# Kernel tuning notes

Hardware: AMD Instinct MI355X
Metric: run time of the kernel (lower is better)

The kernel has to match this reference:

```python
import jax, jax.numpy as jnp
import numpy as np

B, S, D, H = 4, 2048, 1024, 16
DK = D // H

def setup_inputs() -> dict:
    key = jax.random.key(0)
    ks = jax.random.split(key, 5)
    x = jax.random.normal(ks[0], (B, S, D), dtype=jnp.float32)
    scale = 1.0 / np.sqrt(D)
    Wq = jax.random.normal(ks[1], (D, D), dtype=jnp.float32) * scale
    Wk = jax.random.normal(ks[2], (D, D), dtype=jnp.float32) * scale
    Wv = jax.random.normal(ks[3], (D, D), dtype=jnp.float32) * scale
    Wo = jax.random.normal(ks[4], (D, D), dtype=jnp.float32) * scale
    return {"x": x, "Wq": Wq, "Wk": Wk, "Wv": Wv, "Wo": Wo}

def reference(x, Wq, Wk, Wv, Wo):
    # F.linear: y = x @ W.T  (weights stored torch-style [out, in])
    q = jnp.einsum('bsd,ed->bse', x, Wq).reshape(B, S, H, DK).transpose(0, 2, 1, 3)
    k = jnp.einsum('bsd,ed->bse', x, Wk).reshape(B, S, H, DK).transpose(0, 2, 1, 3)
    v = jnp.einsum('bsd,ed->bse', x, Wv).reshape(B, S, H, DK).transpose(0, 2, 1, 3)
    scores = jnp.einsum('bhqd,bhkd->bhqk', q, k) / jnp.sqrt(jnp.float32(DK))
    attn = jax.nn.softmax(scores, axis=-1)  # dropout p=0.0 -> identity
    out = jnp.einsum('bhqk,bhkd->bhqd', attn, v)
    out = out.transpose(0, 2, 1, 3).reshape(B, S, D)
    return jnp.einsum('bsd,ed->bse', out, Wo)
```

## Files before the change

kernel.cpp:

```cpp
#include <hip/hip_runtime.h>
#include <hip/hip_bf16.h>

#define B_ 4
#define S_ 2048
#define D_ 1024
#define H_ 16
#define DK_ 64

typedef __attribute__((ext_vector_type(8))) short short8;
typedef __attribute__((ext_vector_type(4))) float floatx4;
typedef __attribute__((ext_vector_type(16))) float floatx16;

static __device__ __forceinline__ unsigned short f2bf(float f) {
    unsigned int u = __float_as_uint(f);
    u += 0x7fffu + ((u >> 16) & 1u);
    return (unsigned short)(u >> 16);
}

static __device__ __forceinline__ unsigned int pack2bf_fast(float a, float b) {
    unsigned int ua = (__float_as_uint(a) + 0x8000u) >> 16;
    unsigned int ub = (__float_as_uint(b) + 0x8000u) & 0xffff0000u;
    return ua | ub;
}

static __device__ __forceinline__ unsigned int pack2bf(float a, float b) {
    return (unsigned int)f2bf(a) | ((unsigned int)f2bf(b) << 16);
}

__global__ void cast_x_kernel(const float* __restrict__ src,
                              unsigned short* __restrict__ dst, int n4) {
    int i = blockIdx.x * blockDim.x + threadIdx.x;
    if (i < n4) {
        float4 v = ((const float4*)src)[i];
        ushort4 o;
        o.x = f2bf(v.x); o.y = f2bf(v.y); o.z = f2bf(v.z); o.w = f2bf(v.w);
        ((ushort4*)dst)[i] = o;
    }
}

struct Ptr4 {
    const float* s[4];
    unsigned short* d[4];
};

__global__ void cast_w_kernel(Ptr4 p, int n4) {
    int m = blockIdx.y;
    int i = blockIdx.x * blockDim.x + threadIdx.x;
    if (i < n4) {
        float4 v = ((const float4*)p.s[m])[i];
        ushort4 o;
        o.x = f2bf(v.x); o.y = f2bf(v.y); o.z = f2bf(v.z); o.w = f2bf(v.w);
        ((ushort4*)p.d[m])[i] = o;
    }
}

template <typename OutT, bool VT2>
__global__ __launch_bounds__(256) void gemm_bt(
    const unsigned short* __restrict__ A,
    const unsigned short* __restrict__ W0,
    const unsigned short* __restrict__ W1,
    const unsigned short* __restrict__ W2,
    OutT* __restrict__ C0, OutT* __restrict__ C1, OutT* __restrict__ C2,
    int M, int N, int K)
{
    __shared__ __align__(16) unsigned short At[128 * 64];
    __shared__ __align__(16) unsigned short Bt[128 * 64];

    const unsigned short* W = (blockIdx.z == 0) ? W0 : ((blockIdx.z == 1) ? W1 : W2);
    OutT* C = (blockIdx.z == 0) ? C0 : ((blockIdx.z == 1) ? C1 : C2);

    const int n0 = blockIdx.x * 128;
    const int m0 = blockIdx.y * 128;
    const int wv = threadIdx.x >> 6;
    const int ln = threadIdx.x & 63;
    const int quad = ln >> 4;
    const int l15 = ln & 15;
    const int wm = (wv >> 1) * 64;
    const int wn = (wv & 1) * 64;

    floatx4 acc[4][4];
#pragma unroll
    for (int i = 0; i < 4; i++)
#pragma unroll
        for (int j = 0; j < 4; j++) acc[i][j] = floatx4{0.f, 0.f, 0.f, 0.f};

    const int lr = ln >> 3;
    const int lc = (ln & 7) * 8;

    for (int k0 = 0; k0 < K; k0 += 64) {
        __syncthreads();
#pragma unroll
        for (int c = 0; c < 4; c++) {
            int rowA = wv * 32 + c * 8;
            const unsigned short* gA = A + (size_t)(m0 + rowA + lr) * K + k0 + lc;
            __builtin_amdgcn_global_load_lds(
                (const __attribute__((address_space(1))) void*)gA,
                (__attribute__((address_space(3))) void*)&At[rowA * 64], 16, 0, 0);
            const unsigned short* gB = W + (size_t)(n0 + rowA + lr) * K + k0 + lc;
            __builtin_amdgcn_global_load_lds(
                (const __attribute__((address_space(1))) void*)gB,
                (__attribute__((address_space(3))) void*)&Bt[rowA * 64], 16, 0, 0);
        }
        __syncthreads();

#pragma unroll
        for (int kk = 0; kk < 2; kk++) {
            short8 af[4], bf[4];
#pragma unroll
            for (int i = 0; i < 4; i++)
                af[i] = *(const short8*)&At[(wm + i * 16 + l15) * 64 + kk * 32 + quad * 8];
#pragma unroll
            for (int j = 0; j < 4; j++)
                bf[j] = *(const short8*)&Bt[(wn + j * 16 + l15) * 64 + kk * 32 + quad * 8];
#pragma unroll
            for (int i = 0; i < 4; i++)
#pragma unroll
                for (int j = 0; j < 4; j++)
                    acc[i][j] = __builtin_amdgcn_mfma_f32_16x16x32_bf16(af[i], bf[j], acc[i][j], 0, 0, 0);
        }
    }

    if constexpr (VT2) {
        if (blockIdx.z == 2) {
            unsigned short* Vt = (unsigned short*)C;
#pragma unroll
            for (int i = 0; i < 4; i++)
#pragma unroll
                for (int j = 0; j < 4; j++) {
                    int col = n0 + wn + j * 16 + l15;
                    int row0 = m0 + wm + i * 16 + quad * 4;
                    int bb = row0 >> 11, ss = row0 & 2047;
                    size_t addr = ((size_t)(bb * 1024 + col)) * 2048 + ss;
                    uint2 pk;
                    pk.x = pack2bf(acc[i][j][0], acc[i][j][1]);
                    pk.y = pack2bf(acc[i][j][2], acc[i][j][3]);
                    *(uint2*)((unsigned short*)Vt + addr) = pk;
                }
            return;
        }
    }

#pragma unroll
    for (int i = 0; i < 4; i++)
#pragma unroll
        for (int j = 0; j < 4; j++)
#pragma unroll
            for (int r = 0; r < 4; r++) {
                int row = m0 + wm + i * 16 + quad * 4 + r;
                int col = n0 + wn + j * 16 + l15;
                float v = acc[i][j][r];
                if constexpr (sizeof(OutT) == 2)
                    C[(size_t)row * N + col] = (OutT)f2bf(v);
                else
                    C[(size_t)row * N + col] = v;
            }
}

__global__ __launch_bounds__(256, 4) void flash_attn(
    const unsigned short* __restrict__ Q,
    const unsigned short* __restrict__ K,
    const unsigned short* __restrict__ Vt,
    unsigned short* __restrict__ O)
{
    __shared__ __align__(16) unsigned short Kt[64 * 72];
    __shared__ __align__(16) unsigned short VT[64 * 72];
    __shared__ __align__(16) unsigned short Pl[4][32 * 72];

    const int qt = blockIdx.x;
    const int h = blockIdx.y;
    const int b = blockIdx.z;
    const int tid = threadIdx.x;
    const int wv = tid >> 6;
    const int ln = tid & 63;
    const int l31 = ln & 31;
    const int half = ln >> 5;

    const size_t base = ((size_t)b * S_) * D_ + (size_t)h * DK_;
    const size_t vtbase = ((size_t)(b * 1024 + h * 64)) * (size_t)S_;

    const int qrow = qt * 128 + wv * 32 + l31;
    short8 qf[4];
    {
        const unsigned short* qp = Q + base + (size_t)qrow * D_ + half * 8;
#pragma unroll
        for (int ks = 0; ks < 4; ks++) qf[ks] = *(const short8*)(qp + ks * 16);
    }

    floatx16 Oacc[2];
#pragma unroll
    for (int mt = 0; mt < 2; mt++)
#pragma unroll
        for (int e = 0; e < 16; e++) Oacc[mt][e] = 0.f;
    float l_i = 0.f;

    const int srow = tid >> 3;
    const int scol = (tid & 7) * 8;

    const float scl = 1.4426950408889634f / 8.0f;
    const float CL = 12.0f;

    for (int kt = 0; kt < S_ / 64; kt++) {
        __syncthreads();
#pragma unroll
        for (int c = 0; c < 2; c++) {
            int row = srow + c * 32;
            *(short8*)&Kt[row * 72 + scol] =
                *(const short8*)(K + base + (size_t)(kt * 64 + row) * D_ + scol);
            *(short8*)&VT[row * 72 + scol] =
                *(const short8*)(Vt + vtbase + (size_t)row * S_ + kt * 64 + scol);
        }
        __syncthreads();

        floatx16 sac[2];
#pragma unroll
        for (int mt = 0; mt < 2; mt++) {
#pragma unroll
            for (int e = 0; e < 16; e++) sac[mt][e] = 0.f;
#pragma unroll
            for (int ks = 0; ks < 4; ks++) {
                short8 kf = *(const short8*)&Kt[(mt * 32 + l31) * 72 + ks * 16 + half * 8];
                sac[mt] = __builtin_amdgcn_mfma_f32_32x32x16_bf16(kf, qf[ks], sac[mt], 0, 0, 0);
            }
        }

#pragma unroll
        for (int mt = 0; mt < 2; mt++)
#pragma unroll
            for (int g = 0; g < 4; g++) {
                float p0 = __builtin_amdgcn_exp2f(fmaf(sac[mt][4 * g + 0], scl, -CL));
                float p1 = __builtin_amdgcn_exp2f(fmaf(sac[mt][4 * g + 1], scl, -CL));
                float p2 = __builtin_amdgcn_exp2f(fmaf(sac[mt][4 * g + 2], scl, -CL));
                float p3 = __builtin_amdgcn_exp2f(fmaf(sac[mt][4 * g + 3], scl, -CL));
                l_i += (p0 + p1) + (p2 + p3);
                uint2 pk;
                pk.x = pack2bf_fast(p0, p1);
                pk.y = pack2bf_fast(p2, p3);
                *(uint2*)&Pl[wv][l31 * 72 + mt * 32 + 8 * g + 4 * half] = pk;
            }
        asm volatile("s_waitcnt lgkmcnt(0)" ::: "memory");

#pragma unroll
        for (int ks = 0; ks < 4; ks++) {
            short8 pf = *(const short8*)&Pl[wv][l31 * 72 + ks * 16 + half * 8];
#pragma unroll
            for (int mt = 0; mt < 2; mt++) {
                short8 vf = *(const short8*)&VT[(mt * 32 + l31) * 72 + ks * 16 + half * 8];
                Oacc[mt] = __builtin_amdgcn_mfma_f32_32x32x16_bf16(vf, pf, Oacc[mt], 0, 0, 0);
            }
        }
    }

    l_i += __shfl_xor(l_i, 32);
    float inv = 1.0f / l_i;

#pragma unroll
    for (int mt = 0; mt < 2; mt++)
#pragma unroll
        for (int g = 0; g < 4; g++) {
            uint2 pk;
            pk.x = pack2bf(Oacc[mt][4 * g + 0] * inv, Oacc[mt][4 * g + 1] * inv);
            pk.y = pack2bf(Oacc[mt][4 * g + 2] * inv, Oacc[mt][4 * g + 3] * inv);
            *(uint2*)(O + base + (size_t)qrow * D_ + mt * 32 + 8 * g + 4 * half) = pk;
        }
}

extern "C" void kernel_launch(void* const* d_in, const int* in_sizes, int n_in,
                              void* d_out, int out_size, void* d_ws, size_t ws_size,
                              hipStream_t stream) {
    const float* x  = (const float*)d_in[0];
    const float* Wq = (const float*)d_in[1];
    const float* Wk = (const float*)d_in[2];
    const float* Wv = (const float*)d_in[3];
    const float* Wo = (const float*)d_in[4];
    float* out = (float*)d_out;

    char* ws = (char*)d_ws;
    const size_t MB = 1024 * 1024;
    unsigned short* xb  = (unsigned short*)(ws);
    unsigned short* wqb = (unsigned short*)(ws + 16 * MB);
    unsigned short* wkb = (unsigned short*)(ws + 18 * MB);
    unsigned short* wvb = (unsigned short*)(ws + 20 * MB);
    unsigned short* wob = (unsigned short*)(ws + 22 * MB);
    unsigned short* Qb  = (unsigned short*)(ws + 24 * MB);
    unsigned short* Kb  = (unsigned short*)(ws + 40 * MB);
    unsigned short* Vtb = (unsigned short*)(ws + 56 * MB);
    unsigned short* Ob  = (unsigned short*)(ws);

    int nx4 = (B_ * S_ * D_) / 4;
    cast_x_kernel<<<nx4 / 256, 256, 0, stream>>>(x, xb, nx4);

    Ptr4 p4;
    p4.s[0] = Wq; p4.s[1] = Wk; p4.s[2] = Wv; p4.s[3] = Wo;
    p4.d[0] = wqb; p4.d[1] = wkb; p4.d[2] = wvb; p4.d[3] = wob;
    int nw4 = (D_ * D_) / 4;
    cast_w_kernel<<<dim3(nw4 / 256, 4, 1), 256, 0, stream>>>(p4, nw4);

    dim3 gq(D_ / 128, (B_ * S_) / 128, 3);
    gemm_bt<unsigned short, true><<<gq, 256, 0, stream>>>(
        xb, wqb, wkb, wvb, Qb, Kb, Vtb, B_ * S_, D_, D_);

    dim3 gf(S_ / 128, H_, B_);
    flash_attn<<<gf, 256, 0, stream>>>(Qb, Kb, Vtb, Ob);

    dim3 go(D_ / 128, (B_ * S_) / 128, 1);
    gemm_bt<float, false><<<go, 256, 0, stream>>>(
        Ob, wob, wob, wob, out, out, out, B_ * S_, D_, D_);
}
```

Before: 307.1 us.

## Keep softmax P in registers via permlane32 swap and merge cast kernels

Measured after the change: 310.1 us. About the same (+1.0%).

```diff
diff --git a/kernel.cpp b/kernel.cpp
--- a/kernel.cpp
+++ b/kernel.cpp
@@ -10,6 +10,7 @@
 typedef __attribute__((ext_vector_type(8))) short short8;
 typedef __attribute__((ext_vector_type(4))) float floatx4;
 typedef __attribute__((ext_vector_type(16))) float floatx16;
+typedef __attribute__((ext_vector_type(4))) unsigned int uint4v;
 
 static __device__ __forceinline__ unsigned short f2bf(float f) {
     unsigned int u = __float_as_uint(f);
@@ -27,31 +28,32 @@
     return (unsigned int)f2bf(a) | ((unsigned int)f2bf(b) << 16);
 }
 
-__global__ void cast_x_kernel(const float* __restrict__ src,
-                              unsigned short* __restrict__ dst, int n4) {
+#define PLSWAP(a, b) asm volatile("v_permlane32_swap_b32 %0, %1" : "+v"(a), "+v"(b))
+
+struct CastAll {
+    const float* x;
+    const float* w[4];
+    unsigned short* xd;
+    unsigned short* wd[4];
+};
+
+__global__ void cast_all_kernel(CastAll a) {
     int i = blockIdx.x * blockDim.x + threadIdx.x;
-    if (i < n4) {
-        float4 v = ((const float4*)src)[i];
-        ushort4 o;
-        o.x = f2bf(v.x); o.y = f2bf(v.y); o.z = f2bf(v.z); o.w = f2bf(v.w);
-        ((ushort4*)dst)[i] = o;
-    }
-}
-
-struct Ptr4 {
-    const float* s[4];
-    unsigned short* d[4];
-};
-
-__global__ void cast_w_kernel(Ptr4 p, int n4) {
-    int m = blockIdx.y;
-    int i = blockIdx.x * blockDim.x + threadIdx.x;
-    if (i < n4) {
-        float4 v = ((const float4*)p.s[m])[i];
-        ushort4 o;
-        o.x = f2bf(v.x); o.y = f2bf(v.y); o.z = f2bf(v.z); o.w = f2bf(v.w);
-        ((ushort4*)p.d[m])[i] = o;
-    }
+    const float* s;
+    unsigned short* d;
+    int j;
+    if (i < 2097152) {
+        s = a.x; d = a.xd; j = i;
+    } else {
+        int k = i - 2097152;
+        int w = k >> 18;
+        j = k & 262143;
+        s = a.w[w]; d = a.wd[w];
+    }
+    float4 v = ((const float4*)s)[j];
+    ushort4 o;
+    o.x = f2bf(v.x); o.y = f2bf(v.y); o.z = f2bf(v.z); o.w = f2bf(v.w);
+    ((ushort4*)d)[j] = o;
 }
 
 template <typename OutT, bool VT2>
@@ -164,7 +166,6 @@
 {
     __shared__ __align__(16) unsigned short Kt[64 * 72];
     __shared__ __align__(16) unsigned short VT[64 * 72];
-    __shared__ __align__(16) unsigned short Pl[4][32 * 72];
 
     const int qt = blockIdx.x;
     const int h = blockIdx.y;
@@ -223,6 +224,7 @@
             }
         }
 
+        uint2 run[2][4];
 #pragma unroll
         for (int mt = 0; mt < 2; mt++)
 #pragma unroll
@@ -232,22 +234,32 @@
                 float p2 = __builtin_amdgcn_exp2f(fmaf(sac[mt][4 * g + 2], scl, -CL));
                 float p3 = __builtin_amdgcn_exp2f(fmaf(sac[mt][4 * g + 3], scl, -CL));
                 l_i += (p0 + p1) + (p2 + p3);
-                uint2 pk;
-                pk.x = pack2bf_fast(p0, p1);
-                pk.y = pack2bf_fast(p2, p3);
-                *(uint2*)&Pl[wv][l31 * 72 + mt * 32 + 8 * g + 4 * half] = pk;
-            }
-        asm volatile("s_waitcnt lgkmcnt(0)" ::: "memory");
-
-#pragma unroll
-        for (int ks = 0; ks < 4; ks++) {
-            short8 pf = *(const short8*)&Pl[wv][l31 * 72 + ks * 16 + half * 8];
-#pragma unroll
-            for (int mt = 0; mt < 2; mt++) {
-                short8 vf = *(const short8*)&VT[(mt * 32 + l31) * 72 + ks * 16 + half * 8];
-                Oacc[mt] = __builtin_amdgcn_mfma_f32_32x32x16_bf16(vf, pf, Oacc[mt], 0, 0, 0);
-            }
-        }
+                run[mt][g].x = pack2bf_fast(p0, p1);
+                run[mt][g].y = pack2bf_fast(p2, p3);
+            }
+
+#pragma unroll
+        for (int mt = 0; mt < 2; mt++)
+#pragma unroll
+            for (int t = 0; t < 2; t++) {
+                PLSWAP(run[mt][2 * t].x, run[mt][2 * t + 1].x);
+                PLSWAP(run[mt][2 * t].y, run[mt][2 * t + 1].y);
+            }
+
+#pragma unroll
+        for (int mt2 = 0; mt2 < 2; mt2++)
+#pragma unroll
+            for (int t = 0; t < 2; t++) {
+                int ks = mt2 * 2 + t;
+                uint4v u = {run[mt2][2 * t].x, run[mt2][2 * t].y,
+                            run[mt2][2 * t + 1].x, run[mt2][2 * t + 1].y};
+                short8 pf = __builtin_bit_cast(short8, u);
+#pragma unroll
+                for (int mt = 0; mt < 2; mt++) {
+                    short8 vf = *(const short8*)&VT[(mt * 32 + l31) * 72 + ks * 16 + half * 8];
+                    Oacc[mt] = __builtin_amdgcn_mfma_f32_32x32x16_bf16(vf, pf, Oacc[mt], 0, 0, 0);
+                }
+            }
     }
 
     l_i += __shfl_xor(l_i, 32);
@@ -286,14 +298,11 @@
     unsigned short* Vtb = (unsigned short*)(ws + 56 * MB);
     unsigned short* Ob  = (unsigned short*)(ws);
 
-    int nx4 = (B_ * S_ * D_) / 4;
-    cast_x_kernel<<<nx4 / 256, 256, 0, stream>>>(x, xb, nx4);
-
-    Ptr4 p4;
-    p4.s[0] = Wq; p4.s[1] = Wk; p4.s[2] = Wv; p4.s[3] = Wo;
-    p4.d[0] = wqb; p4.d[1] = wkb; p4.d[2] = wvb; p4.d[3] = wob;
-    int nw4 = (D_ * D_) / 4;
-    cast_w_kernel<<<dim3(nw4 / 256, 4, 1), 256, 0, stream>>>(p4, nw4);
+    CastAll ca;
+    ca.x = x; ca.xd = xb;
+    ca.w[0] = Wq; ca.w[1] = Wk; ca.w[2] = Wv; ca.w[3] = Wo;
+    ca.wd[0] = wqb; ca.wd[1] = wkb; ca.wd[2] = wvb; ca.wd[3] = wob;
+    cast_all_kernel<<<12288, 256, 0, stream>>>(ca);
 
     dim3 gq(D_ / 128, (B_ * S_) / 128, 3);
     gemm_bt<unsigned short, true><<<gq, 256, 0, stream>>>(
```
